# Optimization experiments

Hardware: AMD Instinct MI355X
Metric: run time of the kernel (lower is better)

## Reference

```python
import jax, jax.numpy as jnp
import numpy as np

SCALE = 0.125  # 1/sqrt(embed_dim=64), as passed to Self_Attn in the original


def setup_inputs() -> dict:
    key = jax.random.key(0)
    ks = jax.random.split(key, 6)
    B, S, N, D = 8192, 50, 100000, 64
    nodes = jax.random.randint(ks[0], (B,), 0, N)
    node_seq = jax.random.randint(ks[1], (B, S), 0, N)
    uv2e_weight = jax.random.normal(ks[2], (N, D), dtype=jnp.float32)
    feat_weight = jax.random.normal(ks[3], (N, D), dtype=jnp.float32)
    W1 = jax.random.normal(ks[4], (D, 2 * D), dtype=jnp.float32) * 0.05  # torch Linear weight (out, in)
    b1 = jax.random.normal(ks[5], (D,), dtype=jnp.float32) * 0.05
    return {"nodes": nodes, "node_seq": node_seq, "uv2e_weight": uv2e_weight,
            "feat_weight": feat_weight, "W1": W1, "b1": b1}


def reference(nodes, node_seq, uv2e_weight, feat_weight, W1, b1):
    # gather embeddings: q from self ids, k=v from padded/reversed neighbor sequences
    q = uv2e_weight[nodes]          # [B, D]
    k = uv2e_weight[node_seq]       # [B, S, D]
    v = k                           # same gather in the original
    # Self_Attn: scaled dot-product attention, query length 1 per node
    scores = jnp.einsum('bd,bsd->bs', q, k) * SCALE          # [B, S]
    attn = jax.nn.softmax(scores, axis=-1)                   # [B, S]
    folded = jnp.einsum('bs,bsd->bd', attn, v)                # [B, D]
    # self features (features(nodes).t() in torch yields [B, D])
    self_feats = feat_weight[nodes]                           # [B, D]
    combined = jnp.concatenate([self_feats, folded], axis=1)  # [B, 2D]
    out = jax.nn.relu(combined @ W1.T + b1)                   # [B, D]
    return out
```

## Files before the change

kernel.cpp:

```cpp
#include <hip/hip_runtime.h>
#include <hip/hip_bf16.h>
#include <math.h>


#define DD      64
#define SS      50
#define HS      25
#define RPW     2
#define WPB     4
#define RPB     (RPW * WPB)
#define PDEPTH  8
#define SCALE_L2E 0.180336880f

__device__ __forceinline__ float rdlane_f(float v, int l) {
    return __int_as_float(__builtin_amdgcn_readlane(__float_as_int(v), l));
}

template <int CTRL>
__device__ __forceinline__ float dpp_add(float x) {
    int r = __builtin_amdgcn_update_dpp(0, __float_as_int(x), CTRL, 0xf, 0xf, true);
    return x + __int_as_float(r);
}

__global__ __launch_bounds__(256) void folded_encoder_kernel(
    const int*   __restrict__ nodes,
    const int*   __restrict__ node_seq,
    const float* __restrict__ uv2e,
    const float* __restrict__ feat,
    const float* __restrict__ W1,
    const float* __restrict__ b1,
    float*       __restrict__ out,
    int B)
{
    __shared__ __align__(16) float Wsw[DD][2 * DD];
    __shared__ int seqbuf[WPB][RPW * SS];

    const int tid = threadIdx.x;
    const int wid = tid >> 6;
    const int ln  = tid & 63;
    const int rr  = ln >> 5;
    const int h   = (ln >> 4) & 1;
    const int t   = ln & 15;

    const int wrow0 = (blockIdx.x * WPB + wid) * RPW;

    {
        long base = (long)wrow0 * SS;
        seqbuf[wid][ln] = node_seq[base + ln];
        int pos = 64 + ln;
        if (pos < RPW * SS) seqbuf[wid][pos] = node_seq[base + pos];
    }

    #pragma unroll
    for (int rep = 0; rep < 32; ++rep) {
        int e = rep * 256 + tid;
        int o = e >> 7;
        int i = e & 127;
        int c = i >> 2, j = i & 3;
        Wsw[o][(((c ^ (o & 7)) << 2) + j)] = W1[e];
    }

    const int row  = wrow0 + rr;
    const int rowc = row < B ? row : B - 1;
    const int nid  = nodes[rowc];
    const float4 q4 = *(const float4*)(uv2e + (size_t)nid * DD + 4 * t);
    const float4 f4 = *(const float4*)(feat + (size_t)nid * DD + 4 * t);
    const float bias = b1[ln];

    __syncthreads();

    const int* sb = &seqbuf[wid][rr * SS + h * HS];

    float  l   = 0.f;
    float4 acc = make_float4(0.f, 0.f, 0.f, 0.f);
    float4 kq[PDEPTH];

    #pragma unroll
    for (int v = 0; v < PDEPTH; ++v)
        kq[v] = *(const float4*)(uv2e + (size_t)sb[v] * DD + 4 * t);

    #pragma unroll
    for (int s = 0; s < HS; ++s) {
        float4 kk = kq[s % PDEPTH];
        if (s + PDEPTH < HS)
            kq[s % PDEPTH] = *(const float4*)(uv2e + (size_t)sb[s + PDEPTH] * DD + 4 * t);

        float p = kk.x * q4.x + kk.y * q4.y + kk.z * q4.z + kk.w * q4.w;
        p = dpp_add<0xB1>(p);
        p = dpp_add<0x4E>(p);
        p = dpp_add<0x141>(p);
        p = dpp_add<0x140>(p);

        float e = __builtin_amdgcn_exp2f(p * SCALE_L2E);
        l += e;
        acc.x += e * kk.x;
        acc.y += e * kk.y;
        acc.z += e * kk.z;
        acc.w += e * kk.w;
    }

    l     += __shfl_xor(l, 16);
    acc.x += __shfl_xor(acc.x, 16);
    acc.y += __shfl_xor(acc.y, 16);
    acc.z += __shfl_xor(acc.z, 16);
    acc.w += __shfl_xor(acc.w, 16);

    const float rl = __builtin_amdgcn_rcpf(l);
    const float4 fold = make_float4(acc.x * rl, acc.y * rl, acc.z * rl, acc.w * rl);

    float oa[RPW][2];
    #pragma unroll
    for (int r2 = 0; r2 < RPW; ++r2) { oa[r2][0] = bias; oa[r2][1] = 0.f; }

    const float* wrow = &Wsw[ln][0];
    #pragma unroll
    for (int cc = 0; cc < 32; ++cc) {
        float4 w4 = *(const float4*)&wrow[((cc ^ (ln & 7)) << 2)];
        #pragma unroll
        for (int r2 = 0; r2 < RPW; ++r2) {
            const int srcl = r2 * 32 + (cc & 15);
            float c0, c1, c2, c3;
            if (cc < 16) {
                c0 = rdlane_f(f4.x, srcl); c1 = rdlane_f(f4.y, srcl);
                c2 = rdlane_f(f4.z, srcl); c3 = rdlane_f(f4.w, srcl);
            } else {
                c0 = rdlane_f(fold.x, srcl); c1 = rdlane_f(fold.y, srcl);
                c2 = rdlane_f(fold.z, srcl); c3 = rdlane_f(fold.w, srcl);
            }
            oa[r2][cc & 1]       += c0 * w4.x + c1 * w4.y;
            oa[r2][(cc & 1) ^ 1] += c2 * w4.z + c3 * w4.w;
        }
    }

    #pragma unroll
    for (int r2 = 0; r2 < RPW; ++r2) {
        int r = wrow0 + r2;
        if (r < B) {
            float v = oa[r2][0] + oa[r2][1];
            out[(size_t)r * DD + ln] = fmaxf(v, 0.f);
        }
    }
}

extern "C" void kernel_launch(void* const* d_in, const int* in_sizes, int n_in,
                              void* d_out, int out_size, void* d_ws, size_t ws_size,
                              hipStream_t stream) {
    const int*   nodes    = (const int*)  d_in[0];
    const int*   node_seq = (const int*)  d_in[1];
    const float* uv2e     = (const float*)d_in[2];
    const float* feat     = (const float*)d_in[3];
    const float* W1       = (const float*)d_in[4];
    const float* b1       = (const float*)d_in[5];
    float*       out      = (float*)d_out;

    const int B = in_sizes[0];
    const int blocks = (B + RPB - 1) / RPB;

    folded_encoder_kernel<<<blocks, 256, 0, stream>>>(
        nodes, node_seq, uv2e, feat, W1, b1, out, B);
}
```

Before: 110.0 us.

## Gather neighbor keys from an fp16 copy of the embedding table, one row per wave

Each call first converts the whole uv2e table to fp16 in workspace, then gathers neighbor keys from that half-size copy. The softmax-weighted sum is now computed in reduced precision on the keys. The encoder is restructured to one row per wave with four 16-lane groups each handling about 13 neighbors, all loads issued up front, and a 512-thread block. The intent is to halve the bytes of the random key gathers and raise memory-level parallelism. The price is a full-table conversion pass on every call (25.6MB read plus 12.8MB written), which may cost more than it saves on 8192×50 gathers.

```diff
diff --git a/kernel.cpp b/kernel.cpp
--- a/kernel.cpp
+++ b/kernel.cpp
@@ -1,15 +1,11 @@
 #include <hip/hip_runtime.h>
-#include <hip/hip_bf16.h>
+#include <hip/hip_fp16.h>
 #include <math.h>
 
 
 #define DD      64
 #define SS      50
-#define HS      25
-#define RPW     2
-#define WPB     4
-#define RPB     (RPW * WPB)
-#define PDEPTH  8
+#define WPB     8
 #define SCALE_L2E 0.180336880f
 
 __device__ __forceinline__ float rdlane_f(float v, int l) {
@@ -22,124 +18,128 @@
     return x + __int_as_float(r);
 }
 
-__global__ __launch_bounds__(256) void folded_encoder_kernel(
-    const int*   __restrict__ nodes,
-    const int*   __restrict__ node_seq,
-    const float* __restrict__ uv2e,
-    const float* __restrict__ feat,
-    const float* __restrict__ W1,
-    const float* __restrict__ b1,
-    float*       __restrict__ out,
+__global__ __launch_bounds__(256) void cvt_f32_f16_kernel(
+    const float* __restrict__ src, __half* __restrict__ dst, int n8)
+{
+    int i = blockIdx.x * blockDim.x + threadIdx.x;
+    if (i >= n8) return;
+    const float4* s4 = (const float4*)src;
+    float4 a = s4[2 * i];
+    float4 b = s4[2 * i + 1];
+    union { __half h[8]; uint4 u; } o;
+    o.h[0] = __float2half(a.x); o.h[1] = __float2half(a.y);
+    o.h[2] = __float2half(a.z); o.h[3] = __float2half(a.w);
+    o.h[4] = __float2half(b.x); o.h[5] = __float2half(b.y);
+    o.h[6] = __float2half(b.z); o.h[7] = __float2half(b.w);
+    *(uint4*)(dst + 8 * i) = o.u;
+}
+
+__global__ __launch_bounds__(512, 6) void folded_encoder_kernel(
+    const int*    __restrict__ nodes,
+    const int*    __restrict__ node_seq,
+    const float*  __restrict__ uv2e,
+    const float*  __restrict__ feat,
+    const float*  __restrict__ W1,
+    const float*  __restrict__ b1,
+    const __half* __restrict__ ktab,
+    float*        __restrict__ out,
     int B)
 {
     __shared__ __align__(16) float Wsw[DD][2 * DD];
-    __shared__ int seqbuf[WPB][RPW * SS];
+    __shared__ int seqbuf[WPB][SS + 2];
 
     const int tid = threadIdx.x;
     const int wid = tid >> 6;
     const int ln  = tid & 63;
-    const int rr  = ln >> 5;
-    const int h   = (ln >> 4) & 1;
+    const int g   = ln >> 4;
     const int t   = ln & 15;
 
-    const int wrow0 = (blockIdx.x * WPB + wid) * RPW;
-
-    {
-        long base = (long)wrow0 * SS;
-        seqbuf[wid][ln] = node_seq[base + ln];
-        int pos = 64 + ln;
-        if (pos < RPW * SS) seqbuf[wid][pos] = node_seq[base + pos];
-    }
+    const int row  = blockIdx.x * WPB + wid;
+    const int rowc = row < B ? row : B - 1;
 
     #pragma unroll
-    for (int rep = 0; rep < 32; ++rep) {
-        int e = rep * 256 + tid;
+    for (int rep = 0; rep < 16; ++rep) {
+        int e = rep * 512 + tid;
         int o = e >> 7;
         int i = e & 127;
         int c = i >> 2, j = i & 3;
-        Wsw[o][(((c ^ (o & 7)) << 2) + j)] = W1[e];
+        Wsw[o][((c ^ (o & 7)) << 2) + j] = W1[e];
     }
+    if (ln < SS) seqbuf[wid][ln] = node_seq[(size_t)rowc * SS + ln];
 
-    const int row  = wrow0 + rr;
-    const int rowc = row < B ? row : B - 1;
-    const int nid  = nodes[rowc];
+    const int nid = nodes[rowc];
     const float4 q4 = *(const float4*)(uv2e + (size_t)nid * DD + 4 * t);
     const float4 f4 = *(const float4*)(feat + (size_t)nid * DD + 4 * t);
     const float bias = b1[ln];
 
     __syncthreads();
 
-    const int* sb = &seqbuf[wid][rr * SS + h * HS];
+    const int start = (25 * g) >> 1;
+    const int len   = ((25 * (g + 1)) >> 1) - start;
+    const int* sb   = &seqbuf[wid][0];
+
+    int idxr[13];
+    #pragma unroll
+    for (int s = 0; s < 13; ++s)
+        idxr[s] = sb[start + (s < len ? s : 0)];
+
+    uint2 kr[13];
+    #pragma unroll
+    for (int s = 0; s < 13; ++s)
+        kr[s] = *(const uint2*)(ktab + (size_t)idxr[s] * DD + 4 * t);
 
     float  l   = 0.f;
     float4 acc = make_float4(0.f, 0.f, 0.f, 0.f);
-    float4 kq[PDEPTH];
+    #pragma unroll
+    for (int s = 0; s < 13; ++s) {
+        union { uint2 u; __half h[4]; } kw; kw.u = kr[s];
+        float k0 = __half2float(kw.h[0]);
+        float k1 = __half2float(kw.h[1]);
+        float k2 = __half2float(kw.h[2]);
+        float k3 = __half2float(kw.h[3]);
 
-    #pragma unroll
-    for (int v = 0; v < PDEPTH; ++v)
-        kq[v] = *(const float4*)(uv2e + (size_t)sb[v] * DD + 4 * t);
-
-    #pragma unroll
-    for (int s = 0; s < HS; ++s) {
-        float4 kk = kq[s % PDEPTH];
-        if (s + PDEPTH < HS)
-            kq[s % PDEPTH] = *(const float4*)(uv2e + (size_t)sb[s + PDEPTH] * DD + 4 * t);
-
-        float p = kk.x * q4.x + kk.y * q4.y + kk.z * q4.z + kk.w * q4.w;
+        float p = k0 * q4.x + k1 * q4.y + k2 * q4.z + k3 * q4.w;
         p = dpp_add<0xB1>(p);
         p = dpp_add<0x4E>(p);
         p = dpp_add<0x141>(p);
         p = dpp_add<0x140>(p);
 
-        float e = __builtin_amdgcn_exp2f(p * SCALE_L2E);
-        l += e;
-        acc.x += e * kk.x;
-        acc.y += e * kk.y;
-        acc.z += e * kk.z;
-        acc.w += e * kk.w;
+        float e  = __builtin_amdgcn_exp2f(p * SCALE_L2E);
+        float ee = (s < len) ? e : 0.f;
+        l += ee;
+        acc.x += ee * k0; acc.y += ee * k1;
+        acc.z += ee * k2; acc.w += ee * k3;
     }
 
-    l     += __shfl_xor(l, 16);
-    acc.x += __shfl_xor(acc.x, 16);
-    acc.y += __shfl_xor(acc.y, 16);
-    acc.z += __shfl_xor(acc.z, 16);
-    acc.w += __shfl_xor(acc.w, 16);
+    l     += __shfl_xor(l, 16);     l     += __shfl_xor(l, 32);
+    acc.x += __shfl_xor(acc.x, 16); acc.x += __shfl_xor(acc.x, 32);
+    acc.y += __shfl_xor(acc.y, 16); acc.y += __shfl_xor(acc.y, 32);
+    acc.z += __shfl_xor(acc.z, 16); acc.z += __shfl_xor(acc.z, 32);
+    acc.w += __shfl_xor(acc.w, 16); acc.w += __shfl_xor(acc.w, 32);
 
-    const float rl = __builtin_amdgcn_rcpf(l);
+    const float rl = 1.0f / l;
     const float4 fold = make_float4(acc.x * rl, acc.y * rl, acc.z * rl, acc.w * rl);
 
-    float oa[RPW][2];
-    #pragma unroll
-    for (int r2 = 0; r2 < RPW; ++r2) { oa[r2][0] = bias; oa[r2][1] = 0.f; }
-
+    float oa0 = bias, oa1 = 0.f;
     const float* wrow = &Wsw[ln][0];
     #pragma unroll
     for (int cc = 0; cc < 32; ++cc) {
         float4 w4 = *(const float4*)&wrow[((cc ^ (ln & 7)) << 2)];
-        #pragma unroll
-        for (int r2 = 0; r2 < RPW; ++r2) {
-            const int srcl = r2 * 32 + (cc & 15);
-            float c0, c1, c2, c3;
-            if (cc < 16) {
-                c0 = rdlane_f(f4.x, srcl); c1 = rdlane_f(f4.y, srcl);
-                c2 = rdlane_f(f4.z, srcl); c3 = rdlane_f(f4.w, srcl);
-            } else {
-                c0 = rdlane_f(fold.x, srcl); c1 = rdlane_f(fold.y, srcl);
-                c2 = rdlane_f(fold.z, srcl); c3 = rdlane_f(fold.w, srcl);
-            }
-            oa[r2][cc & 1]       += c0 * w4.x + c1 * w4.y;
-            oa[r2][(cc & 1) ^ 1] += c2 * w4.z + c3 * w4.w;
+        const int srcl = cc & 15;
+        float c0, c1, c2, c3;
+        if (cc < 16) {
+            c0 = rdlane_f(f4.x, srcl); c1 = rdlane_f(f4.y, srcl);
+            c2 = rdlane_f(f4.z, srcl); c3 = rdlane_f(f4.w, srcl);
+        } else {
+            c0 = rdlane_f(fold.x, srcl); c1 = rdlane_f(fold.y, srcl);
+            c2 = rdlane_f(fold.z, srcl); c3 = rdlane_f(fold.w, srcl);
         }
+        oa0 += c0 * w4.x + c1 * w4.y;
+        oa1 += c2 * w4.z + c3 * w4.w;
     }
 
-    #pragma unroll
-    for (int r2 = 0; r2 < RPW; ++r2) {
-        int r = wrow0 + r2;
-        if (r < B) {
-            float v = oa[r2][0] + oa[r2][1];
-            out[(size_t)r * DD + ln] = fmaxf(v, 0.f);
-        }
-    }
+    if (row < B)
+        out[(size_t)row * DD + ln] = fmaxf(oa0 + oa1, 0.f);
 }
 
 extern "C" void kernel_launch(void* const* d_in, const int* in_sizes, int n_in,
@@ -152,10 +152,15 @@
     const float* W1       = (const float*)d_in[4];
     const float* b1       = (const float*)d_in[5];
     float*       out      = (float*)d_out;
+    __half*      ktab     = (__half*)d_ws;
 
-    const int B = in_sizes[0];
-    const int blocks = (B + RPB - 1) / RPB;
+    const int B  = in_sizes[0];
+    const int NE = in_sizes[2];
+    const int n8 = NE / 8;
 
-    folded_encoder_kernel<<<blocks, 256, 0, stream>>>(
-        nodes, node_seq, uv2e, feat, W1, b1, out, B);
+    cvt_f32_f16_kernel<<<(n8 + 255) / 256, 256, 0, stream>>>(uv2e, ktab, n8);
+
+    const int blocks = (B + WPB - 1) / WPB;
+    folded_encoder_kernel<<<blocks, 512, 0, stream>>>(
+        nodes, node_seq, uv2e, feat, W1, b1, ktab, out, B);
 }
```

Result: no change. 108.3 us (-1.6%).
